# Kernel optimization log

Measured on AMD Instinct MI355X. Metric: run time of the kernel, lower is better.

The kernel has to match this reference:

```python
import jax, jax.numpy as jnp
import numpy as np

# dims
B, N, T, D = 32, 207, 12, 128
H, HD, L, FF = 8, 16, 4, 512
PL, OD, IN = 12, 1, 1
SCALE = 1.0 / float(np.sqrt(HD))
NEG = -1e9


def ln(x, g, b, eps=1e-5):
    m = jnp.mean(x, -1, keepdims=True)
    v = jnp.mean((x - m) ** 2, -1, keepdims=True)
    return (x - m) * jax.lax.rsqrt(v + eps) * g + b


def setup_inputs() -> dict:
    key = jax.random.key(0)
    keys = iter(jax.random.split(key, 48))
    def rn(shape, s=0.02):
        return jax.random.normal(next(keys), shape, jnp.float32) * s
    z = lambda *s: jnp.zeros(s, jnp.float32)
    o = lambda *s: jnp.ones(s, jnp.float32)
    inp = {
        "x": jax.random.normal(next(keys), (B, N, T, IN), jnp.float32),
        "adj": jax.random.randint(next(keys), (N, N), 0, 2, jnp.int32),
        "Wi": rn((IN, D)), "bi": z(D),
        # spatial blocks (stacked over L layers)
        "Wq": rn((L, D, D)), "Wk": rn((L, D, D)), "Wv": rn((L, D, D)),
        "Wo": rn((L, D, D)), "bo": z(L, D),
        "sW1": rn((L, D, FF)), "sB1": z(L, FF), "sW2": rn((L, FF, D)), "sB2": z(L, D),
        "sg1": o(L, D), "sh1": z(L, D), "sg2": o(L, D), "sh2": z(L, D),
        # temporal blocks
        "Win": rn((L, D, 3 * D)), "Bin": z(L, 3 * D), "Wout": rn((L, D, D)), "Bout": z(L, D),
        "tW1": rn((L, D, FF)), "tB1": z(L, FF), "tW2": rn((L, FF, D)), "tB2": z(L, D),
        "tg1": o(L, D), "th1": z(L, D), "tg2": o(L, D), "th2": z(L, D),
        # prediction head
        "P1": rn((D, 2 * D)), "Pb1": z(2 * D), "P2": rn((2 * D, D)), "Pb2": z(D),
        "P3": rn((D, PL * OD)), "Pb3": z(PL * OD),
    }
    return inp


def reference(x, adj, Wi, bi, Wq, Wk, Wv, Wo, bo, sW1, sB1, sW2, sB2,
              sg1, sh1, sg2, sh2, Win, Bin, Wout, Bout, tW1, tB1, tW2, tB2,
              tg1, th1, tg2, th2, P1, Pb1, P2, Pb2, P3, Pb3):
    mask = (adj == 0)  # [N,N] True = masked (no edge)
    cmask = jnp.triu(jnp.ones((T, T), bool), 1)  # causal mask over time
    h = x @ Wi + bi  # [B,N,T,D]
    for l in range(L):
        # --- spatial adjacency-masked attention (vectorized over t) ---
        xn = ln(h, sg1[l], sh1[l])
        q = (xn @ Wq[l]).reshape(B, N, T, H, HD)
        k = (xn @ Wk[l]).reshape(B, N, T, H, HD)
        v = (xn @ Wv[l]).reshape(B, N, T, H, HD)
        sc = jnp.einsum('bnthd,bmthd->bthnm', q, k) * SCALE  # [B,T,H,N,N]
        sc = jnp.where(mask[None, None, None], NEG, sc)
        a = jax.nn.softmax(sc, -1)
        o = jnp.einsum('bthnm,bmthd->bnthd', a, v).reshape(B, N, T, D)
        h = h + o @ Wo[l] + bo[l]
        xn = ln(h, sg2[l], sh2[l])
        h = h + jax.nn.relu(xn @ sW1[l] + sB1[l]) @ sW2[l] + sB2[l]
        # --- temporal causal attention (per node) ---
        xn = ln(h, tg1[l], th1[l])
        qkv = xn @ Win[l] + Bin[l]
        q, k, v = jnp.split(qkv, 3, -1)
        q = q.reshape(B, N, T, H, HD)
        k = k.reshape(B, N, T, H, HD)
        v = v.reshape(B, N, T, H, HD)
        sc = jnp.einsum('bnthd,bnshd->bnhts', q, k) * SCALE  # [B,N,H,T,T]
        sc = jnp.where(cmask[None, None, None], NEG, sc)
        a = jax.nn.softmax(sc, -1)
        o = jnp.einsum('bnhts,bnshd->bnthd', a, v).reshape(B, N, T, D)
        h = h + o @ Wout[l] + Bout[l]
        xn = ln(h, tg2[l], th2[l])
        h = h + jax.nn.relu(xn @ tW1[l] + tB1[l]) @ tW2[l] + tB2[l]
    # prediction head on last time step
    hl = h[:, :, -1, :]  # [B,N,D]
    zz = jax.nn.relu(hl @ P1 + Pb1)
    zz = jax.nn.relu(zz @ P2 + Pb2)
    return (zz @ P3 + Pb3).reshape(B, N, PL, OD)
```

## Files before the change

kernel.cpp:

```cpp
#include <hip/hip_runtime.h>
#include <hip/hip_bf16.h>

#define B_   32
#define N_   207
#define T_   12
#define D_   128
#define H_   8
#define HD_  16
#define L_   4
#define FF_  512
#define PL_  12
#define TOK  (B_*N_*T_)
#define ROWS2 (B_*N_)
#define SCALE_ 0.25f
#define NEG_  -1e9f
#define NPAD 208
#define KQ2  24
#define KVH  232

typedef __hip_bfloat16 bf16;
typedef unsigned int u32;
typedef __attribute__((ext_vector_type(8))) short bf16x8;
typedef __attribute__((ext_vector_type(8))) _Float16 f16x8;
typedef __attribute__((ext_vector_type(4))) float f32x4;

__device__ __forceinline__ float b2f(bf16 x){ return __bfloat162float(x); }
__device__ __forceinline__ bf16  f2b(float x){ return __float2bfloat16(x); }

__device__ __forceinline__ void gll16(const bf16* g, bf16* l){
  __builtin_amdgcn_global_load_lds((const __attribute__((address_space(1))) void*)g,
                                   (__attribute__((address_space(3))) void*)l, 16, 0, 0);
}

__global__ void detect_k(const void* x, int* flag){
  __shared__ int cnt[256];
  const unsigned short* u = (const unsigned short*)x;
  int ok = 0;
  for (int i = threadIdx.x; i < 4096; i += 256){
    unsigned int bits = ((unsigned int)u[i]) << 16;
    float f = __uint_as_float(bits);
    float a = fabsf(f);
    if (f == 0.0f || (a > 1e-4f && a < 64.0f)) ok++;
  }
  cnt[threadIdx.x] = ok;
  __syncthreads();
  for (int s = 128; s > 0; s >>= 1){
    if (threadIdx.x < s) cnt[threadIdx.x] += cnt[threadIdx.x + s];
    __syncthreads();
  }
  if (threadIdx.x == 0) *flag = (cnt[0] > 3686) ? 1 : 0;
}

struct FlatArgs {
  const void* src[24];
  long long dst[24];
  int cum[25];
};
__global__ void cvt_flat_k(FlatArgs a, bf16* base, const int* flag, int total){
  int i = blockIdx.x*256 + threadIdx.x;
  if (i >= total) return;
  int j = 0;
  while (i >= a.cum[j+1]) j++;
  int loc = i - a.cum[j];
  float v = (*flag) ? b2f(((const bf16*)a.src[j])[loc]) : ((const float*)a.src[j])[loc];
  base[a.dst[j] + loc] = f2b(v);
}

struct TArgs {
  const void* src[10];
  long long dst[10];
  int K[10], Nc[10], Lstr[10], ro[10];
  int cum[11];
};
__global__ void cvt_t_k(TArgs a, bf16* base, const int* flag, int total){
  int i = blockIdx.x*256 + threadIdx.x;
  if (i >= total) return;
  int j = 0;
  while (i >= a.cum[j+1]) j++;
  int loc = i - a.cum[j];
  int KN = a.K[j]*a.Nc[j];
  int l = loc / KN; int rm = loc - l*KN; int k = rm / a.Nc[j]; int n = rm - k*a.Nc[j];
  float v = (*flag) ? b2f(((const bf16*)a.src[j])[loc]) : ((const float*)a.src[j])[loc];
  base[a.dst[j] + (long long)l*a.Lstr[j] + (long long)(a.ro[j]+n)*a.K[j] + k] = f2b(v);
}

__global__ void abits_k(const int* adj, u32* out){
  int i = blockIdx.x*256 + threadIdx.x;
  if (i >= NPAD*7) return;
  int n = i / 7, wj = i % 7;
  u32 v = 0;
  if (n < N_){
    for (int bit = 0; bit < 32; bit++){
      int m = wj*32 + bit;
      if (m < N_ && adj[n*N_ + m] != 0) v |= (1u << bit);
    }
  }
  out[i] = v;
}

__global__ void embed_ln_k(const bf16* x, const bf16* Wi, const bf16* bi,
                           const bf16* g, const bf16* bta, float* h, bf16* xnb){
  int wave = threadIdx.x >> 6, lane = threadIdx.x & 63;
  int tok = blockIdx.x*4 + wave;
  if (tok >= TOK) return;
  float xv = b2f(x[tok]);
  float v0 = xv*b2f(Wi[lane])    + b2f(bi[lane]);
  float v1 = xv*b2f(Wi[lane+64]) + b2f(bi[lane+64]);
  float* hp = h + (size_t)tok*D_;
  hp[lane] = v0; hp[lane+64] = v1;
  float s = v0 + v1;
  for (int off = 32; off >= 1; off >>= 1) s += __shfl_xor(s, off, 64);
  float m = s * (1.0f/128.0f);
  float d0 = v0 - m, d1 = v1 - m;
  float vv = d0*d0 + d1*d1;
  for (int off = 32; off >= 1; off >>= 1) vv += __shfl_xor(vv, off, 64);
  float r = rsqrtf(vv*(1.0f/128.0f) + 1e-5f);
  bf16* op = xnb + (size_t)tok*D_;
  op[lane]    = f2b(d0*r*b2f(g[lane])    + b2f(bta[lane]));
  op[lane+64] = f2b(d1*r*b2f(g[lane+64]) + b2f(bta[lane+64]));
}

__global__ __launch_bounds__(256) void mgemm_k(const bf16* __restrict__ A,
    const bf16* __restrict__ Wt, const bf16* __restrict__ bias,
    bf16* __restrict__ outp, int ldo, int Ktot, int relu){
  __shared__ __align__(16) bf16 As[128*32];
  __shared__ __align__(16) bf16 Bs[128*32];
  int tid = threadIdx.x;
  int rowBase = blockIdx.y * 128, colBase = blockIdx.x * 128;
  int w = tid >> 6, lane = tid & 63, quad = lane >> 4, cl = lane & 15;
  int waveM = w >> 1, waveN = w & 1;
  f32x4 accr[4][4];
  #pragma unroll
  for (int i = 0; i < 4; i++)
    #pragma unroll
    for (int j = 0; j < 4; j++) accr[i][j] = (f32x4){0.f,0.f,0.f,0.f};
  int lr = tid >> 2, kc = tid & 3;
  const bf16* Ap = A  + (size_t)(rowBase + lr)*Ktot + kc*8;
  const bf16* Bp = Wt + (size_t)(colBase + lr)*Ktot + kc*8;
  bf16* AsW = As + tid*8;
  bf16* BsW = Bs + tid*8;
  for (int kk = 0; kk < Ktot; kk += 32){
    __syncthreads();
    gll16(Ap + kk, AsW);
    gll16(Ap + (size_t)64*Ktot + kk, AsW + 64*32);
    gll16(Bp + kk, BsW);
    gll16(Bp + (size_t)64*Ktot + kk, BsW + 64*32);
    __syncthreads();
    bf16x8 af[4], bfr[4];
    #pragma unroll
    for (int mi = 0; mi < 4; mi++)
      af[mi] = *(const bf16x8*)(As + (waveM*64 + mi*16 + cl)*32 + quad*8);
    #pragma unroll
    for (int nj = 0; nj < 4; nj++)
      bfr[nj] = *(const bf16x8*)(Bs + (waveN*64 + nj*16 + cl)*32 + quad*8);
    #pragma unroll
    for (int mi = 0; mi < 4; mi++)
      #pragma unroll
      for (int nj = 0; nj < 4; nj++)
        accr[mi][nj] = __builtin_amdgcn_mfma_f32_16x16x32_bf16(af[mi], bfr[nj], accr[mi][nj], 0,0,0);
  }
  float bv[4];
  #pragma unroll
  for (int nj = 0; nj < 4; nj++)
    bv[nj] = bias ? b2f(bias[colBase + waveN*64 + nj*16 + cl]) : 0.0f;
  #pragma unroll
  for (int mi = 0; mi < 4; mi++){
    int row0 = rowBase + waveM*64 + mi*16 + quad*4;
    #pragma unroll
    for (int nj = 0; nj < 4; nj++){
      int col = colBase + waveN*64 + nj*16 + cl;
      #pragma unroll
      for (int r = 0; r < 4; r++){
        float v = accr[mi][nj][r] + bv[nj];
        if (relu) v = fmaxf(v, 0.0f);
        outp[(size_t)(row0+r)*ldo + col] = f2b(v);
      }
    }
  }
}

__global__ __launch_bounds__(256) void mgemm_ln_k(const bf16* __restrict__ A,
    const bf16* __restrict__ Wt, const bf16* __restrict__ bias,
    float* __restrict__ hout, int Ktot,
    const bf16* __restrict__ g, const bf16* __restrict__ bta,
    bf16* __restrict__ xnb){
  __shared__ __align__(16) bf16 As[128*32];
  __shared__ __align__(16) bf16 Bs[128*32];
  __shared__ float red[2][128][2];
  int tid = threadIdx.x;
  int rowBase = blockIdx.y * 128;
  int w = tid >> 6, lane = tid & 63, quad = lane >> 4, cl = lane & 15;
  int waveM = w >> 1, waveN = w & 1;
  f32x4 accr[4][4];
  #pragma unroll
  for (int i = 0; i < 4; i++)
    #pragma unroll
    for (int j = 0; j < 4; j++) accr[i][j] = (f32x4){0.f,0.f,0.f,0.f};
  int lr = tid >> 2, kc = tid & 3;
  const bf16* Ap = A  + (size_t)(rowBase + lr)*Ktot + kc*8;
  const bf16* Bp = Wt + (size_t)lr*Ktot + kc*8;
  bf16* AsW = As + tid*8;
  bf16* BsW = Bs + tid*8;
  for (int kk = 0; kk < Ktot; kk += 32){
    __syncthreads();
    gll16(Ap + kk, AsW);
    gll16(Ap + (size_t)64*Ktot + kk, AsW + 64*32);
    gll16(Bp + kk, BsW);
    gll16(Bp + (size_t)64*Ktot + kk, BsW + 64*32);
    __syncthreads();
    bf16x8 af[4], bfr[4];
    #pragma unroll
    for (int mi = 0; mi < 4; mi++)
      af[mi] = *(const bf16x8*)(As + (waveM*64 + mi*16 + cl)*32 + quad*8);
    #pragma unroll
    for (int nj = 0; nj < 4; nj++)
      bfr[nj] = *(const bf16x8*)(Bs + (waveN*64 + nj*16 + cl)*32 + quad*8);
    #pragma unroll
    for (int mi = 0; mi < 4; mi++)
      #pragma unroll
      for (int nj = 0; nj < 4; nj++)
        accr[mi][nj] = __builtin_amdgcn_mfma_f32_16x16x32_bf16(af[mi], bfr[nj], accr[mi][nj], 0,0,0);
  }
  int colW = waveN*64;
  float bv[4];
  #pragma unroll
  for (int nj = 0; nj < 4; nj++)
    bv[nj] = bias ? b2f(bias[colW + nj*16 + cl]) : 0.0f;
  float hv[4][4][4];
  float psum[4][4], psq[4][4];
  #pragma unroll
  for (int mi = 0; mi < 4; mi++)
    #pragma unroll
    for (int r = 0; r < 4; r++){ psum[mi][r] = 0.f; psq[mi][r] = 0.f; }
  #pragma unroll
  for (int mi = 0; mi < 4; mi++){
    #pragma unroll
    for (int r = 0; r < 4; r++){
      int row = rowBase + waveM*64 + mi*16 + quad*4 + r;
      #pragma unroll
      for (int nj = 0; nj < 4; nj++){
        int col = colW + nj*16 + cl;
        size_t idx = (size_t)row*D_ + col;
        float v = hout[idx] + accr[mi][nj][r] + bv[nj];
        hout[idx] = v;
        hv[mi][nj][r] = v;
        psum[mi][r] += v; psq[mi][r] += v*v;
      }
    }
  }
  if (g){
    #pragma unroll
    for (int off = 1; off <= 8; off <<= 1)
      #pragma unroll
      for (int mi = 0; mi < 4; mi++)
        #pragma unroll
        for (int r = 0; r < 4; r++){
          psum[mi][r] += __shfl_xor(psum[mi][r], off, 64);
          psq[mi][r]  += __shfl_xor(psq[mi][r],  off, 64);
        }
    if (cl == 0){
      #pragma unroll
      for (int mi = 0; mi < 4; mi++)
        #pragma unroll
        for (int r = 0; r < 4; r++){
          int rl = waveM*64 + mi*16 + quad*4 + r;
          red[waveN][rl][0] = psum[mi][r];
          red[waveN][rl][1] = psq[mi][r];
        }
    }
    __syncthreads();
    float gv[4], btv[4];
    #pragma unroll
    for (int nj = 0; nj < 4; nj++){
      int col = colW + nj*16 + cl;
      gv[nj] = b2f(g[col]); btv[nj] = b2f(bta[col]);
    }
    #pragma unroll
    for (int mi = 0; mi < 4; mi++){
      #pragma unroll
      for (int r = 0; r < 4; r++){
        int rl = waveM*64 + mi*16 + quad*4 + r;
        float s = red[0][rl][0] + red[1][rl][0];
        float q = red[0][rl][1] + red[1][rl][1];
        float mean = s*(1.0f/128.0f);
        float var  = q*(1.0f/128.0f) - mean*mean;
        float rstd = rsqrtf(var + 1e-5f);
        int row = rowBase + rl;
        #pragma unroll
        for (int nj = 0; nj < 4; nj++){
          int col = colW + nj*16 + cl;
          xnb[(size_t)row*D_ + col] = f2b((hv[mi][nj][r]-mean)*rstd*gv[nj] + btv[nj]);
        }
      }
    }
  }
}

__global__ __launch_bounds__(256,3) void sattn_k(const bf16* __restrict__ qkv,
    const u32* __restrict__ abg, bf16* __restrict__ ob){
  __shared__ __align__(16) bf16     Ks[NPAD*KQ2];
  __shared__ __align__(16) _Float16 Vt[16*KVH];
  __shared__ __align__(16) _Float16 Ps[4*16*KVH];
  __shared__ u32 abs_[NPAD*7];
  int tid = threadIdx.x;
  int bid = blockIdx.x;
  int b = bid / (T_*H_); int rem = bid % (T_*H_); int t = rem / H_; int hh = rem % H_;
  for (int i = tid; i < 16*25; i += 256){ int d = i/25, c = 207 + i%25; Vt[d*KVH + c] = (_Float16)0.0f; }
  for (int i = tid; i < 64*24; i += 256){ int row = i/24, c = 208 + i%24; Ps[row*KVH + c] = (_Float16)0.0f; }
  for (int i = tid; i < N_*16; i += 256){
    int n = i >> 4, d = i & 15;
    size_t rowb = ((size_t)((b*N_ + n)*T_ + t))*384 + hh*HD_;
    Ks[n*KQ2 + d] = qkv[rowb + 128 + d];
    Vt[d*KVH + n] = (_Float16)b2f(qkv[rowb + 256 + d]);
  }
  for (int i = tid; i < NPAD*7; i += 256) abs_[i] = abg[i];
  __syncthreads();

  int w = tid >> 6, lane = tid & 63, quad = lane >> 4, cl = lane & 15;
  int nstripes = (w == 0) ? 4 : 3;
  for (int si = 0; si < nstripes; si++){
    int mi = w + si*4;
    bf16x8 aq = (bf16x8){0,0,0,0,0,0,0,0};
    {
      int n = mi*16 + cl; if (n > N_-1) n = N_-1;
      size_t rowb = ((size_t)((b*N_ + n)*T_ + t))*384 + hh*HD_;
      if (quad < 2) aq = *(const bf16x8*)(qkv + rowb + quad*8);
    }
    f32x4 s[13];
    #pragma unroll
    for (int nj = 0; nj < 13; nj++){
      bf16x8 bk = (bf16x8){0,0,0,0,0,0,0,0};
      if (quad < 2) bk = *(const bf16x8*)(Ks + (nj*16 + cl)*KQ2 + quad*8);
      f32x4 z = {0.f,0.f,0.f,0.f};
      s[nj] = __builtin_amdgcn_mfma_f32_16x16x32_bf16(aq, bk, z, 0,0,0);
    }
    int row0 = mi*16 + quad*4;
    _Float16* Pw = Ps + w*16*KVH;
    #pragma unroll
    for (int r = 0; r < 4; r++){
      const u32* ab = abs_ + (row0 + r)*7;
      float mx = -3.4e38f;
      #pragma unroll
      for (int nj = 0; nj < 13; nj++){
        int cg = nj*16 + cl;
        float v = s[nj][r] * SCALE_;
        if (cg > 206) v = -3.4e38f;
        else if (!((ab[cg >> 5] >> (cg & 31)) & 1)) v = NEG_;
        s[nj][r] = v;
        mx = fmaxf(mx, v);
      }
      for (int off = 1; off < 16; off <<= 1) mx = fmaxf(mx, __shfl_xor(mx, off, 64));
      float sum = 0.0f;
      #pragma unroll
      for (int nj = 0; nj < 13; nj++){
        float e = __expf(s[nj][r] - mx);
        s[nj][r] = e; sum += e;
      }
      for (int off = 1; off < 16; off <<= 1) sum += __shfl_xor(sum, off, 64);
      float inv = 1.0f/sum;
      _Float16* Pr = Pw + (quad*4 + r)*KVH;
      #pragma unroll
      for (int nj = 0; nj < 13; nj++) Pr[nj*16 + cl] = (_Float16)(s[nj][r]*inv);
    }
    __threadfence_block();
    f32x4 o = {0.f,0.f,0.f,0.f};
    #pragma unroll
    for (int kt = 0; kt < 7; kt++){
      f16x8 ap = *(const f16x8*)(Pw + cl*KVH + kt*32 + quad*8);
      f16x8 bv = *(const f16x8*)(Vt + cl*KVH + kt*32 + quad*8);
      o = __builtin_amdgcn_mfma_f32_16x16x32_f16(ap, bv, o, 0,0,0);
    }
    #pragma unroll
    for (int r = 0; r < 4; r++){
      int rg = row0 + r;
      if (rg < N_)
        ob[((size_t)((b*N_ + rg)*T_ + t))*D_ + hh*HD_ + cl] = f2b(o[r]);
    }
    __threadfence_block();
  }
}

__global__ void tattn_k(const bf16* qkv, bf16* ob){
  int bid = blockIdx.x; int b = bid / N_, n = bid % N_;
  __shared__ float qs[T_*D_];
  __shared__ float ks[T_*D_];
  __shared__ float vs[T_*D_];
  size_t rowb = ((size_t)(b*N_+n)*T_)*384;
  const u32* src = (const u32*)(qkv + rowb);
  for (int idx = threadIdx.x; idx < T_*192; idx += 128){
    int tt = idx / 192, cw = idx - tt*192;
    u32 pr = src[tt*192 + cw];
    union { u32 u; bf16 b[2]; } cv; cv.u = pr;
    float v0 = b2f(cv.b[0]), v1 = b2f(cv.b[1]);
    int arr = cw >> 6, cp2 = (cw & 63)*2;
    float* dst = (arr == 0) ? qs : (arr == 1) ? ks : vs;
    dst[tt*128 + cp2] = v0; dst[tt*128 + cp2 + 1] = v1;
  }
  __syncthreads();
  int p = threadIdx.x;
  if (p < H_*T_){
    int hh = p / T_, t = p - hh*T_;
    float qreg[16];
    for (int d = 0; d < 16; d++) qreg[d] = qs[t*128 + hh*16 + d];
    float sc[12]; float mx = -3.4e38f;
    for (int s = 0; s < 12; s++){
      float a = 0.0f;
      for (int d = 0; d < 16; d++) a += qreg[d]*ks[s*128 + hh*16 + d];
      a = (s <= t) ? a*SCALE_ : -3.4e38f;
      sc[s] = a; mx = fmaxf(mx, a);
    }
    float ssum = 0.0f;
    for (int s = 0; s < 12; s++){
      float e = (s <= t) ? __expf(sc[s]-mx) : 0.0f;
      sc[s] = e; ssum += e;
    }
    float inv = 1.0f/ssum;
    size_t obase = ((size_t)(b*N_+n)*T_ + t)*D_ + hh*16;
    for (int d = 0; d < 16; d++){
      float acc = 0.0f;
      for (int s = 0; s < 12; s++) acc += sc[s]*vs[s*128 + hh*16 + d];
      ob[obase + d] = f2b(acc*inv);
    }
  }
}

__global__ void gemm_k(const bf16* A, int lda, const bf16* W, const bf16* bias,
                       void* outp, int ldo, int M, int Ncols, int K, int relu, int acc){
  __shared__ float Ast[16*68];
  __shared__ float Ws [16*68];
  int tx = threadIdx.x & 15, ty = threadIdx.x >> 4;
  int rowBase = blockIdx.y * 64, colBase = blockIdx.x * 64;
  float accr[4][4];
  for (int i = 0; i < 4; i++) for (int j = 0; j < 4; j++) accr[i][j] = 0.0f;
  for (int kk = 0; kk < K; kk += 16){
    int kq = threadIdx.x & 15, r0 = threadIdx.x >> 4;
    for (int it = 0; it < 4; it++){
      int r = r0 + it*16, row = rowBase + r;
      float v = 0.0f;
      if (row < M) v = b2f(A[(size_t)row*lda + kk + kq]);
      Ast[kq*68 + r] = v;
    }
    int c = threadIdx.x & 63, w0 = threadIdx.x >> 6;
    for (int it = 0; it < 4; it++){
      int kr = w0 + it*4;
      Ws[kr*68 + c] = b2f(W[(size_t)(kk+kr)*Ncols + colBase + c]);
    }
    __syncthreads();
    for (int k = 0; k < 16; k++){
      float av[4], wv[4];
      for (int i = 0; i < 4; i++) av[i] = Ast[k*68 + ty*4 + i];
      for (int j = 0; j < 4; j++) wv[j] = Ws[k*68 + tx*4 + j];
      for (int i = 0; i < 4; i++)
        for (int j = 0; j < 4; j++) accr[i][j] += av[i]*wv[j];
    }
    __syncthreads();
  }
  for (int i = 0; i < 4; i++){
    int row = rowBase + ty*4 + i;
    if (row >= M) continue;
    for (int j = 0; j < 4; j++){
      int col = colBase + tx*4 + j;
      float v = accr[i][j];
      if (bias) v += b2f(bias[col]);
      if (relu) v = fmaxf(v, 0.0f);
      if (acc) ((float*)outp)[(size_t)row*ldo + col] += v;
      else     ((bf16*)outp)[(size_t)row*ldo + col] = f2b(v);
    }
  }
}

__global__ void gather_k(const float* h, bf16* hlb){
  int i = blockIdx.x*256 + threadIdx.x;
  if (i >= ROWS2*D_) return;
  int r = i >> 7, d = i & 127;
  hlb[i] = f2b(h[((size_t)r*T_ + (T_-1))*D_ + d]);
}

__global__ void head3_k(const bf16* z2, const bf16* P3, const bf16* Pb3,
                        void* out, int out_n, const int* flag){
  int i = blockIdx.x*256 + threadIdx.x;
  if (i >= out_n) return;
  int r = i / PL_, j = i - r*PL_;
  float acc = b2f(Pb3[j]);
  for (int d = 0; d < 128; d++) acc += b2f(z2[(size_t)r*128 + d]) * b2f(P3[d*PL_ + j]);
  if (*flag) ((bf16*)out)[i] = f2b(acc);
  else       ((float*)out)[i] = acc;
}

extern "C" void kernel_launch(void* const* d_in, const int* in_sizes, int n_in,
                              void* d_out, int out_size, void* d_ws, size_t ws_size,
                              hipStream_t stream){
  size_t HB = (size_t)TOK*D_*4;
  size_t XB = (size_t)TOK*D_*2;
  size_t RB = (size_t)TOK*D_*8;
  float* h    = (float*)d_ws;
  bf16*  xnb  = (bf16*)((char*)d_ws + HB);
  bf16*  reg_ = (bf16*)((char*)d_ws + HB + XB);
  bf16*  cvt  = (bf16*)((char*)d_ws + HB + XB + RB);
  bf16*  wsb  = (bf16*)d_ws;
  const int FIDX[34] = {0,2,3,4,5,6,7,8,9,10,11,12,13,14,15,16,17,18,19,20,
                        21,22,23,24,25,26,27,28,29,30,31,32,33,34};
  bf16* cp[34];
  size_t off = 0;
  for (int i = 0; i < 34; i++){ cp[i] = cvt + off; off += (size_t)in_sizes[FIDX[i]]; }
  char* tail   = (char*)d_ws + HB + XB + RB + ((off*2 + 255) & ~(size_t)255);
  u32*  abg    = (u32*)tail;
  bf16* qkvw   = (bf16*)(tail + 8192);
  int*  flag   = (int*)(tail + 8192 + (size_t)L_*384*128*2);

  const bf16 *x_c=cp[0], *Wi_c=cp[1], *bi_c=cp[2],
             *Wo_t=cp[6], *bo_c=cp[7], *sW1_t=cp[8], *sB1_c=cp[9], *sW2_t=cp[10], *sB2_c=cp[11],
             *sg1_c=cp[12], *sh1_c=cp[13], *sg2_c=cp[14], *sh2_c=cp[15], *Win_t=cp[16], *Bin_c=cp[17],
             *Wout_t=cp[18], *Bout_c=cp[19], *tW1_t=cp[20], *tB1_c=cp[21], *tW2_t=cp[22], *tB2_c=cp[23],
             *tg1_c=cp[24], *th1_c=cp[25], *tg2_c=cp[26], *th2_c=cp[27], *P1_c=cp[28], *Pb1_c=cp[29],
             *P2_c=cp[30], *Pb2_c=cp[31], *P3_c=cp[32], *Pb3_c=cp[33];
  const int* adj = (const int*)d_in[1];

  bf16* qkvb = reg_;
  bf16* ob   = reg_ + (size_t)TOK*384;
  bf16* ffb  = reg_;

  detect_k<<<1, 256, 0, stream>>>(d_in[0], flag);

  {
    const int FLAT[24] = {0,1,2,7,9,11,12,13,14,15,17,19,21,23,24,25,26,27,28,29,30,31,32,33};
    FlatArgs fa; int c = 0;
    for (int ii = 0; ii < 24; ii++){
      int ci = FLAT[ii];
      fa.src[ii] = d_in[FIDX[ci]];
      fa.dst[ii] = (long long)(cp[ci] - wsb);
      fa.cum[ii] = c;
      c += in_sizes[FIDX[ci]];
    }
    fa.cum[24] = c;
    cvt_flat_k<<<(c+255)/256, 256, 0, stream>>>(fa, wsb, flag, c);
  }
  {
    TArgs ta; int c = 0;
    const void* srcs[10] = {d_in[4], d_in[5], d_in[6], d_in[7], d_in[9], d_in[11],
                            d_in[17], d_in[19], d_in[21], d_in[23]};
    bf16* dsts[10] = {qkvw, qkvw, qkvw, cp[6], cp[8], cp[10], cp[16], cp[18], cp[20], cp[22]};
    int Ks_[10]   = {128,128,128, 128, 128, 512, 128, 128, 128, 512};
    int Ncs[10]   = {128,128,128, 128, 512, 128, 384, 128, 512, 128};
    int Lst[10]   = {384*128,384*128,384*128, 128*128, 128*512, 512*128, 128*384, 128*128, 128*512, 512*128};
    int ros[10]   = {0,128,256, 0,0,0, 0,0,0, 0};
    for (int j = 0; j < 10; j++){
      ta.src[j] = srcs[j];
      ta.dst[j] = (long long)(dsts[j] - wsb);
      ta.K[j] = Ks_[j]; ta.Nc[j] = Ncs[j]; ta.Lstr[j] = Lst[j]; ta.ro[j] = ros[j];
      ta.cum[j] = c;
      c += L_*Ks_[j]*Ncs[j];
    }
    ta.cum[10] = c;
    cvt_t_k<<<(c+255)/256, 256, 0, stream>>>(ta, wsb, flag, c);
  }
  abits_k<<<(NPAD*7+255)/256, 256, 0, stream>>>(adj, abg);
  embed_ln_k<<<TOK/4, 256, 0, stream>>>(x_c, Wi_c, bi_c, sg1_c, sh1_c, h, xnb);

  const dim3 gP  (1, TOK/128);
  const dim3 gF1 (4, TOK/128);
  const dim3 gQKV(3, TOK/128);

  for (int l = 0; l < L_; l++){
    mgemm_k<<<gQKV, 256, 0, stream>>>(xnb, qkvw + (size_t)l*384*128, nullptr, qkvb, 384, D_, 0);
    sattn_k<<<B_*T_*H_, 256, 0, stream>>>(qkvb, abg, ob);
    mgemm_ln_k<<<gP, 256, 0, stream>>>(ob, Wo_t + (size_t)l*D_*D_, bo_c + l*D_, h, D_,
                                       sg2_c + l*D_, sh2_c + l*D_, xnb);
    mgemm_k<<<gF1, 256, 0, stream>>>(xnb, sW1_t + (size_t)l*D_*FF_, sB1_c + l*FF_, ffb, FF_, D_, 1);
    mgemm_ln_k<<<gP, 256, 0, stream>>>(ffb, sW2_t + (size_t)l*FF_*D_, sB2_c + l*D_, h, FF_,
                                       tg1_c + l*D_, th1_c + l*D_, xnb);
    mgemm_k<<<gQKV, 256, 0, stream>>>(xnb, Win_t + (size_t)l*D_*384, Bin_c + l*384, qkvb, 384, D_, 0);
    tattn_k<<<B_*N_, 128, 0, stream>>>(qkvb, ob);
    mgemm_ln_k<<<gP, 256, 0, stream>>>(ob, Wout_t + (size_t)l*D_*D_, Bout_c + l*D_, h, D_,
                                       tg2_c + l*D_, th2_c + l*D_, xnb);
    mgemm_k<<<gF1, 256, 0, stream>>>(xnb, tW1_t + (size_t)l*D_*FF_, tB1_c + l*FF_, ffb, FF_, D_, 1);
    const bf16* gnext = (l < L_-1) ? (sg1_c + (l+1)*D_) : nullptr;
    const bf16* bnext = (l < L_-1) ? (sh1_c + (l+1)*D_) : nullptr;
    mgemm_ln_k<<<gP, 256, 0, stream>>>(ffb, tW2_t + (size_t)l*FF_*D_, tB2_c + l*D_, h, FF_,
                                       gnext, bnext, xnb);
  }

  bf16* hlb = reg_;
  bf16* z1  = reg_ + (size_t)ROWS2*128;
  bf16* z2  = z1   + (size_t)ROWS2*256;
  gather_k<<<(ROWS2*D_)/256, 256, 0, stream>>>(h, hlb);
  gemm_k<<<dim3(256/64, (ROWS2+63)/64), 256, 0, stream>>>(hlb, 128, P1_c, Pb1_c, z1, 256, ROWS2, 256, 128, 1, 0);
  gemm_k<<<dim3(128/64, (ROWS2+63)/64), 256, 0, stream>>>(z1, 256, P2_c, Pb2_c, z2, 128, ROWS2, 128, 256, 1, 0);
  head3_k<<<(out_size+255)/256, 256, 0, stream>>>(z2, P3_c, Pb3_c, d_out, out_size, flag);
}
```

Measured before the change: 1.767 ms.

## Write spatial QKV into per-(b,t,head) slabs and fold attention scale into Wq

A new QKV GEMM variant scatters Q, K and V into contiguous per-(batch,time,head) slabs of 207x16 elements, so the spatial attention kernel loads K with vector reads and Q/V from contiguous memory instead of strided 384-wide token rows. The 1/sqrt(HD) scale is folded into Wq during weight conversion, which removes the per-score multiply, and the padding-column check is simplified. The cost is a scattered 2-byte store pattern in the GEMM epilogue, which may coalesce poorly, and a separate buffer layout for ob.

```diff
diff --git a/kernel.cpp b/kernel.cpp
--- a/kernel.cpp
+++ b/kernel.cpp
@@ -17,6 +17,7 @@
 #define NPAD 208
 #define KQ2  24
 #define KVH  232
+#define SLAB 3312
 
 typedef __hip_bfloat16 bf16;
 typedef unsigned int u32;
@@ -70,6 +71,7 @@
   const void* src[10];
   long long dst[10];
   int K[10], Nc[10], Lstr[10], ro[10];
+  float scale[10];
   int cum[11];
 };
 __global__ void cvt_t_k(TArgs a, bf16* base, const int* flag, int total){
@@ -81,7 +83,7 @@
   int KN = a.K[j]*a.Nc[j];
   int l = loc / KN; int rm = loc - l*KN; int k = rm / a.Nc[j]; int n = rm - k*a.Nc[j];
   float v = (*flag) ? b2f(((const bf16*)a.src[j])[loc]) : ((const float*)a.src[j])[loc];
-  base[a.dst[j] + (long long)l*a.Lstr[j] + (long long)(a.ro[j]+n)*a.K[j] + k] = f2b(v);
+  base[a.dst[j] + (long long)l*a.Lstr[j] + (long long)(a.ro[j]+n)*a.K[j] + k] = f2b(v*a.scale[j]);
 }
 
 __global__ void abits_k(const int* adj, u32* out){
@@ -179,6 +181,65 @@
   }
 }
 
+__global__ __launch_bounds__(256) void mgemm_qkvT_k(const bf16* __restrict__ A,
+    const bf16* __restrict__ Wt, bf16* __restrict__ sQ,
+    bf16* __restrict__ sK, bf16* __restrict__ sV){
+  __shared__ __align__(16) bf16 As[128*32];
+  __shared__ __align__(16) bf16 Bs[128*32];
+  const int Ktot = 128;
+  int tid = threadIdx.x;
+  int rowBase = blockIdx.y * 128, colBase = blockIdx.x * 128;
+  int w = tid >> 6, lane = tid & 63, quad = lane >> 4, cl = lane & 15;
+  int waveM = w >> 1, waveN = w & 1;
+  f32x4 accr[4][4];
+  #pragma unroll
+  for (int i = 0; i < 4; i++)
+    #pragma unroll
+    for (int j = 0; j < 4; j++) accr[i][j] = (f32x4){0.f,0.f,0.f,0.f};
+  int lr = tid >> 2, kc = tid & 3;
+  const bf16* Ap = A  + (size_t)(rowBase + lr)*Ktot + kc*8;
+  const bf16* Bp = Wt + (size_t)(colBase + lr)*Ktot + kc*8;
+  bf16* AsW = As + tid*8;
+  bf16* BsW = Bs + tid*8;
+  for (int kk = 0; kk < Ktot; kk += 32){
+    __syncthreads();
+    gll16(Ap + kk, AsW);
+    gll16(Ap + (size_t)64*Ktot + kk, AsW + 64*32);
+    gll16(Bp + kk, BsW);
+    gll16(Bp + (size_t)64*Ktot + kk, BsW + 64*32);
+    __syncthreads();
+    bf16x8 af[4], bfr[4];
+    #pragma unroll
+    for (int mi = 0; mi < 4; mi++)
+      af[mi] = *(const bf16x8*)(As + (waveM*64 + mi*16 + cl)*32 + quad*8);
+    #pragma unroll
+    for (int nj = 0; nj < 4; nj++)
+      bfr[nj] = *(const bf16x8*)(Bs + (waveN*64 + nj*16 + cl)*32 + quad*8);
+    #pragma unroll
+    for (int mi = 0; mi < 4; mi++)
+      #pragma unroll
+      for (int nj = 0; nj < 4; nj++)
+        accr[mi][nj] = __builtin_amdgcn_mfma_f32_16x16x32_bf16(af[mi], bfr[nj], accr[mi][nj], 0,0,0);
+  }
+  #pragma unroll
+  for (int mi = 0; mi < 4; mi++){
+    #pragma unroll
+    for (int r = 0; r < 4; r++){
+      int tok = rowBase + waveM*64 + mi*16 + quad*4 + r;
+      int bn = tok / T_; int t = tok - bn*T_;
+      int b = bn / N_;  int n = bn - b*N_;
+      size_t base = ((size_t)(b*T_ + t)*H_)*SLAB + n*16 + cl;
+      #pragma unroll
+      for (int nj = 0; nj < 4; nj++){
+        int col = colBase + waveN*64 + nj*16;
+        int part = col >> 7, hh = (col >> 4) & 7;
+        bf16* dst = (part == 0) ? sQ : (part == 1) ? sK : sV;
+        dst[base + (size_t)hh*SLAB] = f2b(accr[mi][nj][r]);
+      }
+    }
+  }
+}
+
 __global__ __launch_bounds__(256) void mgemm_ln_k(const bf16* __restrict__ A,
     const bf16* __restrict__ Wt, const bf16* __restrict__ bias,
     float* __restrict__ hout, int Ktot,
@@ -296,7 +357,8 @@
   }
 }
 
-__global__ __launch_bounds__(256,3) void sattn_k(const bf16* __restrict__ qkv,
+__global__ __launch_bounds__(256,3) void sattn_k(const bf16* __restrict__ sQ,
+    const bf16* __restrict__ sK, const bf16* __restrict__ sV,
     const u32* __restrict__ abg, bf16* __restrict__ ob){
   __shared__ __align__(16) bf16     Ks[NPAD*KQ2];
   __shared__ __align__(16) _Float16 Vt[16*KVH];
@@ -304,27 +366,32 @@
   __shared__ u32 abs_[NPAD*7];
   int tid = threadIdx.x;
   int bid = blockIdx.x;
-  int b = bid / (T_*H_); int rem = bid % (T_*H_); int t = rem / H_; int hh = rem % H_;
+  int hh = bid & 7; int bt = bid >> 3; int t = bt % T_; int b = bt / T_;
+  const bf16* Kslab = sK + (size_t)bid*SLAB;
+  const bf16* Vslab = sV + (size_t)bid*SLAB;
+  const bf16* Qslab = sQ + (size_t)bid*SLAB;
   for (int i = tid; i < 16*25; i += 256){ int d = i/25, c = 207 + i%25; Vt[d*KVH + c] = (_Float16)0.0f; }
   for (int i = tid; i < 64*24; i += 256){ int row = i/24, c = 208 + i%24; Ps[row*KVH + c] = (_Float16)0.0f; }
-  for (int i = tid; i < N_*16; i += 256){
+  for (int c = tid; c < 414; c += 256){
+    bf16x8 kv = *(const bf16x8*)(Kslab + c*8);
+    int n = c >> 1, dh = (c & 1)*8;
+    *(bf16x8*)(Ks + n*KQ2 + dh) = kv;
+  }
+  for (int i = tid; i < SLAB; i += 256){
     int n = i >> 4, d = i & 15;
-    size_t rowb = ((size_t)((b*N_ + n)*T_ + t))*384 + hh*HD_;
-    Ks[n*KQ2 + d] = qkv[rowb + 128 + d];
-    Vt[d*KVH + n] = (_Float16)b2f(qkv[rowb + 256 + d]);
+    Vt[d*KVH + n] = (_Float16)b2f(Vslab[i]);
   }
   for (int i = tid; i < NPAD*7; i += 256) abs_[i] = abg[i];
   __syncthreads();
 
-  int w = tid >> 6, lane = tid & 63, quad = lane >> 4, cl = lane & 15;
+  int lane = tid & 63, w = tid >> 6, quad = lane >> 4, cl = lane & 15;
   int nstripes = (w == 0) ? 4 : 3;
   for (int si = 0; si < nstripes; si++){
     int mi = w + si*4;
     bf16x8 aq = (bf16x8){0,0,0,0,0,0,0,0};
     {
       int n = mi*16 + cl; if (n > N_-1) n = N_-1;
-      size_t rowb = ((size_t)((b*N_ + n)*T_ + t))*384 + hh*HD_;
-      if (quad < 2) aq = *(const bf16x8*)(qkv + rowb + quad*8);
+      if (quad < 2) aq = *(const bf16x8*)(Qslab + n*16 + quad*8);
     }
     f32x4 s[13];
     #pragma unroll
@@ -343,8 +410,8 @@
       #pragma unroll
       for (int nj = 0; nj < 13; nj++){
         int cg = nj*16 + cl;
-        float v = s[nj][r] * SCALE_;
-        if (cg > 206) v = -3.4e38f;
+        float v = s[nj][r];
+        if (nj == 12 && cl == 15) v = -3.4e38f;
         else if (!((ab[cg >> 5] >> (cg & 31)) & 1)) v = NEG_;
         s[nj][r] = v;
         mx = fmaxf(mx, v);
@@ -516,8 +583,11 @@
              *P2_c=cp[30], *Pb2_c=cp[31], *P3_c=cp[32], *Pb3_c=cp[33];
   const int* adj = (const int*)d_in[1];
 
+  bf16* sQ   = reg_;
+  bf16* sK   = reg_ + (size_t)TOK*128;
+  bf16* sV   = reg_ + (size_t)2*TOK*128;
+  bf16* ob   = reg_ + (size_t)3*TOK*128;
   bf16* qkvb = reg_;
-  bf16* ob   = reg_ + (size_t)TOK*384;
   bf16* ffb  = reg_;
 
   detect_k<<<1, 256, 0, stream>>>(d_in[0], flag);
@@ -548,6 +618,7 @@
       ta.src[j] = srcs[j];
       ta.dst[j] = (long long)(dsts[j] - wsb);
       ta.K[j] = Ks_[j]; ta.Nc[j] = Ncs[j]; ta.Lstr[j] = Lst[j]; ta.ro[j] = ros[j];
+      ta.scale[j] = (j == 0) ? SCALE_ : 1.0f;
       ta.cum[j] = c;
       c += L_*Ks_[j]*Ncs[j];
     }
@@ -562,8 +633,8 @@
   const dim3 gQKV(3, TOK/128);
 
   for (int l = 0; l < L_; l++){
-    mgemm_k<<<gQKV, 256, 0, stream>>>(xnb, qkvw + (size_t)l*384*128, nullptr, qkvb, 384, D_, 0);
-    sattn_k<<<B_*T_*H_, 256, 0, stream>>>(qkvb, abg, ob);
+    mgemm_qkvT_k<<<gQKV, 256, 0, stream>>>(xnb, qkvw + (size_t)l*384*128, sQ, sK, sV);
+    sattn_k<<<B_*T_*H_, 256, 0, stream>>>(sQ, sK, sV, abg, ob);
     mgemm_ln_k<<<gP, 256, 0, stream>>>(ob, Wo_t + (size_t)l*D_*D_, bo_c + l*D_, h, D_,
                                        sg2_c + l*D_, sh2_c + l*D_, xnb);
     mgemm_k<<<gF1, 256, 0, stream>>>(xnb, sW1_t + (size_t)l*D_*FF_, sB1_c + l*FF_, ffb, FF_, D_, 1);
```

Result: no change. 1.751 ms (-0.9%).
